# Kernel optimization log

Measured on AMD Instinct MI355X. Metric: run time of the kernel, lower is better.

Reference implementation:

```python
import jax, jax.numpy as jnp
import numpy as np

B, S, IN, OUT = 32, 128, 64, 64

def setup_inputs() -> dict:
    key = jax.random.key(0)
    ks = jax.random.split(key, 8)
    sc = 0.02
    return {
        "h":  jax.random.normal(ks[0], (B, S, IN), dtype=jnp.float32),
        "W0": jax.random.normal(ks[1], (IN, 2 * IN), dtype=jnp.float32) * sc,  # NN0 weight
        "b0": jax.random.normal(ks[2], (IN,), dtype=jnp.float32) * sc,
        "Ws": jax.random.normal(ks[3], (IN, IN), dtype=jnp.float32) * sc,      # NN0_self weight
        "bs": jax.random.normal(ks[4], (IN,), dtype=jnp.float32) * sc,
        "W1": jax.random.normal(ks[5], (OUT, S * IN), dtype=jnp.float32) * sc, # NN1 weight
        "b1": jax.random.normal(ks[6], (OUT,), dtype=jnp.float32) * sc,
    }

def reference(h, W0, b0, Ws, bs, W1, b1):
    # NN0(cat(h_i, h_j)) = h_i @ W0a.T + h_j @ W0b.T + b0, with W0 = [W0a | W0b]
    W0a, W0b = W0[:, :IN], W0[:, IN:]
    A = jnp.einsum('bsi,oi->bso', h, W0a)            # [B,S,IN] contribution of s1
    C = jnp.einsum('bsi,oi->bso', h, W0b)            # [B,S,IN] contribution of s2
    pair = A[:, :, None, :] + C[:, None, :, :] + b0  # [B,S,S,IN] all (s1,s2) messages
    # diagonal s1 == s2 uses the self network instead
    self_term = jnp.einsum('bsi,oi->bso', h, Ws) + bs  # [B,S,IN]
    idx = jnp.arange(S)
    pair = pair.at[:, idx, idx, :].set(self_term)
    # aggregate: concat over s2 then NN1 -> [B,S,OUT]
    agg = pair.reshape(B, S, S * IN)
    return jnp.einsum('bsk,ok->bso', agg, W1) + b1
```

## Files before the change

### kernel.cpp

```cpp
#include <hip/hip_runtime.h>

#define B   32
#define S   128
#define IN  64
#define ROWS (B*S)
#define K1  (S*IN)

__device__ __forceinline__ int rfl(int x) { return __builtin_amdgcn_readfirstlane(x); }

__global__ __launch_bounds__(256, 2) void prep_kernel(
    const float* __restrict__ h,  const float* __restrict__ W0,
    const float* __restrict__ b0, const float* __restrict__ Ws,
    const float* __restrict__ bs, const float* __restrict__ W1,
    float* __restrict__ U1T, float* __restrict__ Ab,
    float* __restrict__ Df,  float* __restrict__ C)
{
    const int bid  = blockIdx.x;
    const int tid  = threadIdx.x;
    const int lane = tid & 63;
    const int w    = rfl(tid >> 6);

    const int row0 = bid * 8 + w * 2;
    const float4* w0row = (const float4*)(W0 + (size_t)lane * 128);
    const float4* wsrow = (const float4*)(Ws + (size_t)lane * 64);

    float a[2] = {0,0}, c[2] = {0,0}, sf[2] = {0,0};
    #pragma unroll
    for (int ic = 0; ic < 4; ++ic) {
        const int i0 = ic * 16;
        float wa[16], wb[16], wsv[16];
        #pragma unroll
        for (int q = 0; q < 4; ++q) {
            const float4 va = w0row[ic * 4 + q];
            const float4 vb = w0row[16 + ic * 4 + q];
            const float4 vs = wsrow[ic * 4 + q];
            wa [q*4] = va.x; wa [q*4+1] = va.y; wa [q*4+2] = va.z; wa [q*4+3] = va.w;
            wb [q*4] = vb.x; wb [q*4+1] = vb.y; wb [q*4+2] = vb.z; wb [q*4+3] = vb.w;
            wsv[q*4] = vs.x; wsv[q*4+1] = vs.y; wsv[q*4+2] = vs.z; wsv[q*4+3] = vs.w;
        }
        #pragma unroll
        for (int r = 0; r < 2; ++r) {
            const float* hp = h + (size_t)(row0 + r) * 64 + i0;
            #pragma unroll
            for (int j = 0; j < 16; ++j) {
                const float hv = hp[j];
                a [r] += hv * wa [j];
                c [r] += hv * wb [j];
                sf[r] += hv * wsv[j];
            }
        }
    }
    const float b0v = b0[lane], bsv = bs[lane];
    #pragma unroll
    for (int r = 0; r < 2; ++r) {
        const int row = row0 + r;
        const float ab = a[r] + b0v;
        Ab[row * 64 + lane] = ab;
        C [row * 64 + lane] = c[r];
        Df[row * 64 + lane] = sf[r] + bsv - ab - c[r];
    }

    const int g   = bid * 8 + (tid >> 5);
    const int o2  = g >> 6, o = g & 63;
    const int sub = tid & 31;
    float acc = 0.f;
    #pragma unroll
    for (int u = 0; u < 4; ++u)
        acc += W1[(size_t)o2 * K1 + (sub + 32 * u) * 64 + o];
    #pragma unroll
    for (int m = 16; m; m >>= 1) acc += __shfl_xor(acc, m);
    if (sub == 0) U1T[o * 64 + o2] = acc;
}

__global__ __launch_bounds__(256, 2) void dmid_kernel(
    const float* __restrict__ C, const float* __restrict__ W1,
    float* __restrict__ D)
{
    const int bid  = blockIdx.x;
    const int tid  = threadIdx.x;
    const int lane = tid & 63;
    const int w    = rfl(tid >> 6);

    const int g  = bid * 4 + w;
    const int b  = g >> 6, o2 = g & 63;

    const float4* wrow = (const float4*)(W1 + (size_t)o2 * K1) + lane;
    const float4* crow = (const float4*)(C  + (size_t)b  * K1) + lane;

    float s0 = 0, s1 = 0, s2 = 0, s3 = 0;
    #pragma unroll
    for (int j = 0; j < 32; ++j) {
        const float4 w4 = wrow[j * 64];
        const float4 c4 = crow[j * 64];
        s0 += c4.x * w4.x; s1 += c4.y * w4.y;
        s2 += c4.z * w4.z; s3 += c4.w * w4.w;
    }
    float acc = (s0 + s1) + (s2 + s3);
    #pragma unroll
    for (int m = 32; m; m >>= 1) acc += __shfl_xor(acc, m);
    if (lane == 0) D[g] = acc;
}

__global__ __launch_bounds__(256, 4) void final_kernel(
    const float* __restrict__ W1, const float* __restrict__ b1,
    const float* __restrict__ U1T, const float* __restrict__ Ab,
    const float* __restrict__ Df,  const float* __restrict__ D,
    float* __restrict__ out)
{
    const int bid  = blockIdx.x;
    const int tid  = threadIdx.x;
    const int lane = tid & 63;
    const int w    = rfl(tid >> 6);

    const int s = bid >> 3, q = bid & 7;
    const int b = q * 4 + w;

    float acc = D[b * 64 + lane] + b1[lane];

    #pragma unroll
    for (int hh = 0; hh < 2; ++hh) {
        const int o0 = hh * 32;
        float u[32], wc[32];
        #pragma unroll
        for (int j = 0; j < 32; ++j)
            u[j] = U1T[(o0 + j) * 64 + lane];
        const float4* wrow = (const float4*)(W1 + (size_t)lane * K1 + s * 64 + o0);
        #pragma unroll
        for (int qq = 0; qq < 8; ++qq) {
            const float4 v = wrow[qq];
            wc[qq*4] = v.x; wc[qq*4+1] = v.y; wc[qq*4+2] = v.z; wc[qq*4+3] = v.w;
        }
        const float* ap = Ab + ((size_t)(b * S + s)) * 64 + o0;
        const float* dp = Df + ((size_t)(b * S + s)) * 64 + o0;
        float t0 = 0.f;
        #pragma unroll
        for (int j = 0; j < 32; ++j)
            t0 += ap[j] * u[j] + dp[j] * wc[j];
        acc += t0;
    }

    out[((size_t)(b * S + s)) * 64 + lane] = acc;
}

extern "C" void kernel_launch(void* const* d_in, const int* in_sizes, int n_in,
                              void* d_out, int out_size, void* d_ws, size_t ws_size,
                              hipStream_t stream)
{
    const float* h  = (const float*)d_in[0];
    const float* W0 = (const float*)d_in[1];
    const float* b0 = (const float*)d_in[2];
    const float* Ws = (const float*)d_in[3];
    const float* bs = (const float*)d_in[4];
    const float* W1 = (const float*)d_in[5];
    const float* b1 = (const float*)d_in[6];
    float* out = (float*)d_out;

    float* ws  = (float*)d_ws;
    float* U1T = ws;
    float* Ab  = U1T + 64 * 64;
    float* Df  = Ab  + ROWS * 64;
    float* C   = Df  + ROWS * 64;
    float* D   = C   + ROWS * 64;

    prep_kernel <<<512,  256, 0, stream>>>(h, W0, b0, Ws, bs, W1, U1T, Ab, Df, C);
    dmid_kernel <<<512,  256, 0, stream>>>(C, W1, D);
    final_kernel<<<1024, 256, 0, stream>>>(W1, b1, U1T, Ab, Df, D, out);
}
```

Baseline: 37.31 us.

## Transpose W1 in prep kernel for coalesced final-kernel loads; remap dmid grid

The prep kernel now also writes a transposed copy of W1 (W1T, k-major with output index innermost) to the workspace. The final kernel reads its diagonal weight slice from W1T so that lanes read consecutive addresses, replacing the strided float4 reads across W1 rows. The dmid kernel's block-to-(b,o2) mapping is reordered so neighbouring waves share a W1 row, and D is written with the matching index. The transpose costs an extra 2 MB scattered write in prep plus a re-read, in exchange for coalesced access in the final kernel.

```diff
diff --git a/kernel.cpp b/kernel.cpp
--- a/kernel.cpp
+++ b/kernel.cpp
@@ -12,8 +12,9 @@
     const float* __restrict__ h,  const float* __restrict__ W0,
     const float* __restrict__ b0, const float* __restrict__ Ws,
     const float* __restrict__ bs, const float* __restrict__ W1,
-    float* __restrict__ U1T, float* __restrict__ Ab,
-    float* __restrict__ Df,  float* __restrict__ C)
+    float* __restrict__ U1T, float* __restrict__ W1T,
+    float* __restrict__ Ab,  float* __restrict__ Df,
+    float* __restrict__ C)
 {
     const int bid  = blockIdx.x;
     const int tid  = threadIdx.x;
@@ -60,16 +61,30 @@
         Df[row * 64 + lane] = sf[r] + bsv - ab - c[r];
     }
 
-    const int g   = bid * 8 + (tid >> 5);
-    const int o2  = g >> 6, o = g & 63;
-    const int sub = tid & 31;
-    float acc = 0.f;
-    #pragma unroll
-    for (int u = 0; u < 4; ++u)
-        acc += W1[(size_t)o2 * K1 + (sub + 32 * u) * 64 + o];
-    #pragma unroll
-    for (int m = 16; m; m >>= 1) acc += __shfl_xor(acc, m);
-    if (sub == 0) U1T[o * 64 + o2] = acc;
+    {
+        const int g   = bid * 8 + (tid >> 5);
+        const int o2  = g >> 6, o = g & 63;
+        const int sub = tid & 31;
+        float acc = 0.f;
+        #pragma unroll
+        for (int u = 0; u < 4; ++u)
+            acc += W1[(size_t)o2 * K1 + (sub + 32 * u) * 64 + o];
+        #pragma unroll
+        for (int m = 16; m; m >>= 1) acc += __shfl_xor(acc, m);
+        if (sub == 0) U1T[o * 64 + o2] = acc;
+    }
+
+    {
+        const int g2 = bid * 4 + w;
+        const int r2 = g2 >> 5;
+        const int ch = g2 & 31;
+        const float4 wv = *(const float4*)(W1 + (size_t)r2 * K1 + ch * 256 + lane * 4);
+        const size_t kbase = (size_t)(ch * 256 + lane * 4);
+        W1T[(kbase + 0) * 64 + r2] = wv.x;
+        W1T[(kbase + 1) * 64 + r2] = wv.y;
+        W1T[(kbase + 2) * 64 + r2] = wv.z;
+        W1T[(kbase + 3) * 64 + r2] = wv.w;
+    }
 }
 
 __global__ __launch_bounds__(256, 2) void dmid_kernel(
@@ -82,7 +97,7 @@
     const int w    = rfl(tid >> 6);
 
     const int g  = bid * 4 + w;
-    const int b  = g >> 6, o2 = g & 63;
+    const int o2 = g >> 5, b = g & 31;
 
     const float4* wrow = (const float4*)(W1 + (size_t)o2 * K1) + lane;
     const float4* crow = (const float4*)(C  + (size_t)b  * K1) + lane;
@@ -98,12 +113,12 @@
     float acc = (s0 + s1) + (s2 + s3);
     #pragma unroll
     for (int m = 32; m; m >>= 1) acc += __shfl_xor(acc, m);
-    if (lane == 0) D[g] = acc;
+    if (lane == 0) D[b * 64 + o2] = acc;
 }
 
 __global__ __launch_bounds__(256, 4) void final_kernel(
-    const float* __restrict__ W1, const float* __restrict__ b1,
-    const float* __restrict__ U1T, const float* __restrict__ Ab,
+    const float* __restrict__ b1,  const float* __restrict__ U1T,
+    const float* __restrict__ W1T, const float* __restrict__ Ab,
     const float* __restrict__ Df,  const float* __restrict__ D,
     float* __restrict__ out)
 {
@@ -124,12 +139,9 @@
         #pragma unroll
         for (int j = 0; j < 32; ++j)
             u[j] = U1T[(o0 + j) * 64 + lane];
-        const float4* wrow = (const float4*)(W1 + (size_t)lane * K1 + s * 64 + o0);
         #pragma unroll
-        for (int qq = 0; qq < 8; ++qq) {
-            const float4 v = wrow[qq];
-            wc[qq*4] = v.x; wc[qq*4+1] = v.y; wc[qq*4+2] = v.z; wc[qq*4+3] = v.w;
-        }
+        for (int j = 0; j < 32; ++j)
+            wc[j] = W1T[(size_t)(s * 64 + o0 + j) * 64 + lane];
         const float* ap = Ab + ((size_t)(b * S + s)) * 64 + o0;
         const float* dp = Df + ((size_t)(b * S + s)) * 64 + o0;
         float t0 = 0.f;
@@ -157,12 +169,14 @@
 
     float* ws  = (float*)d_ws;
     float* U1T = ws;
-    float* Ab  = U1T + 64 * 64;
+    float* W1T = U1T + 64 * 64;
+    float* Ab  = W1T + K1 * 64;
     float* Df  = Ab  + ROWS * 64;
     float* C   = Df  + ROWS * 64;
     float* D   = C   + ROWS * 64;
 
-    prep_kernel <<<512,  256, 0, stream>>>(h, W0, b0, Ws, bs, W1, U1T, Ab, Df, C);
+    prep_kernel <<<512,  256, 0, stream>>>(h, W0, b0, Ws, bs, W1,
+                                           U1T, W1T, Ab, Df, C);
     dmid_kernel <<<512,  256, 0, stream>>>(C, W1, D);
-    final_kernel<<<1024, 256, 0, stream>>>(W1, b1, U1T, Ab, Df, D, out);
+    final_kernel<<<1024, 256, 0, stream>>>(b1, U1T, W1T, Ab, Df, D, out);
 }
```

Measured after the change: 37.04 us. No clear change (-0.7%).
